# Optimization experiments

Hardware: AMD Instinct MI355X
Metric: run time of the kernel (lower is better)

The kernel has to match this reference:

```python
import jax, jax.numpy as jnp
import numpy as np

MARGIN = 0.3


def setup_inputs() -> dict:
    key = jax.random.key(0)
    k1, k2 = jax.random.split(key)
    N, D, C = 8192, 512, 1024
    embeddings = jax.random.normal(k1, (N, D), dtype=jnp.float32)
    labels = jax.random.randint(k2, (N,), 0, C, dtype=jnp.int64)
    return {"embeddings": embeddings, "labels": labels}


def reference(embeddings, labels):
    # L2-normalize rows, cosine distance via Gram matrix: d = 1 - e_i . e_j
    e = embeddings / jnp.linalg.norm(embeddings, axis=1, keepdims=True)
    dist = 1.0 - jnp.matmul(e, e.T)  # [N, N]

    same = labels[:, None] == labels[None, :]           # [N, N] bool
    eye = jnp.eye(labels.shape[0], dtype=bool)
    pos_mask = same & ~eye                              # positives exclude self
    neg_mask = ~same                                    # negatives

    # Batch-hard mining: hardest (farthest) positive, hardest (closest) negative
    hardest_pos = jnp.max(jnp.where(pos_mask, dist, -jnp.inf), axis=1)
    hardest_neg = jnp.min(jnp.where(neg_mask, dist, jnp.inf), axis=1)

    loss = jax.nn.relu(hardest_pos - hardest_neg + MARGIN)
    return jnp.mean(loss)
```

## Files before the change

kernel.cpp:

```cpp
#include <hip/hip_runtime.h>
#include <hip/hip_fp8.h>
#include <hip/hip_fp16.h>
#include <stdint.h>

#define MARGIN 0.3f

constexpr int N = 8192;
constexpr int D = 512;
constexpr int BM = 128, BN = 128;
constexpr int NKS = D / 64;
constexpr int NT = N / BM;
constexpr int NPAIR = NT * (NT + 1) / 2;
constexpr int WEDGE = NPAIR / 8;
constexpr float ESCALE = 16.0f;
constexpr float INV_SC2 = 1.0f / (ESCALE * ESCALE);

typedef int i32x8 __attribute__((ext_vector_type(8)));
typedef float f32x16 __attribute__((ext_vector_type(16)));
typedef __fp16 h2 __attribute__((ext_vector_type(2)));

constexpr unsigned INF2 = 0x7C007C00u;

__device__ __forceinline__ unsigned char f2fp8(float f) {
  return __hip_fp8_e4m3(f).__x;
}

__device__ __forceinline__ unsigned pkmin(unsigned a, unsigned b) {
  unsigned d;
  asm("v_pk_min_f16 %0, %1, %2" : "=v"(d) : "v"(a), "v"(b));
  return d;
}

__device__ __forceinline__ unsigned cvtpk(float lo, float hi) {
  union { h2 h; unsigned u; } cv;
  cv.h = __builtin_amdgcn_cvt_pkrtz(lo, hi);
  return cv.u;
}

__device__ __forceinline__ void pair_from_q(int q, int& ti, int& tj) {
  int SI = 0;
  while (32 * (SI + 1) * (SI + 1) + 4 * (SI + 1) <= q) ++SI;
  int r = q - (32 * SI * SI + 4 * SI);
  int i, j, SJ;
  if (r < 64 * SI) {
    SJ = r >> 6;
    int w = r & 63;
    i = w >> 3;
    j = w & 7;
  } else {
    int d = r - 64 * SI;
    SJ = SI;
    i = 0;
    while ((i + 1) * (i + 2) / 2 <= d) ++i;
    j = d - i * (i + 1) / 2;
  }
  ti = SI * 8 + i;
  tj = SJ * 8 + j;
}


__global__ __launch_bounds__(256) void normalize_rows(
    const float* __restrict__ emb, unsigned char* __restrict__ e8,
    float* __restrict__ out) {
  if (blockIdx.x == 0 && threadIdx.x == 0) out[0] = 0.f;
  const int wave = threadIdx.x >> 6, lane = threadIdx.x & 63;
  const int row = blockIdx.x * 4 + wave;
  const float4* src = (const float4*)(emb + (size_t)row * D);
  float4 x0 = src[lane];
  float4 x1 = src[lane + 64];
  float ss = x0.x * x0.x + x0.y * x0.y + x0.z * x0.z + x0.w * x0.w +
             x1.x * x1.x + x1.y * x1.y + x1.z * x1.z + x1.w * x1.w;
#pragma unroll
  for (int m = 1; m < 64; m <<= 1) ss += __shfl_xor(ss, m, 64);
  const float r = rsqrtf(ss) * ESCALE;
  union { unsigned char b[8]; uint2 u; } o;
  o.b[0] = f2fp8(x0.x * r); o.b[1] = f2fp8(x0.y * r);
  o.b[2] = f2fp8(x0.z * r); o.b[3] = f2fp8(x0.w * r);
  o.b[4] = f2fp8(x1.x * r); o.b[5] = f2fp8(x1.y * r);
  o.b[6] = f2fp8(x1.z * r); o.b[7] = f2fp8(x1.w * r);
  const int n = row & 31;
  const unsigned inner =
      ((unsigned)(n * 64 + ((lane >> 1) & 3) * 16) ^
       ((unsigned)((n >> 1) & 7) << 4)) + (lane & 1) * 8;
  const unsigned off = (unsigned)((row >> 5) * 8 + (lane >> 3)) * 2048 + inner;
  *(uint2*)(e8 + off) = o.u;
}

__global__ __launch_bounds__(256, 3) void bh_gemm_sym(
    const unsigned char* __restrict__ e8, const int* __restrict__ labels,
    unsigned* __restrict__ scr) {
  __shared__ unsigned char lds[2][16384];
  __shared__ unsigned bufR[2][128];
  __shared__ unsigned bufC[2][128];

  const int b = blockIdx.x;
  const int q = WEDGE * (b & 7) + (b >> 3);
  int ti, tj;
  pair_from_q(q, ti, tj);
  const int iBase = ti * BM, jBase = tj * BN;
  const bool diag = (ti == tj);

  const int tid = threadIdx.x;
  const int lane = tid & 63;
  const int wave = tid >> 6;
  const int wr = wave >> 1, wc = wave & 1;
  const int n = lane & 31, hi = lane >> 5;

  const unsigned o0 =
      (unsigned)(n * 64 + hi * 32) ^ ((unsigned)((n >> 1) & 7) << 4);

  const unsigned char* gsrc[4];
  unsigned ldst[4];
#pragma unroll
  for (int j = 0; j < 4; ++j) {
    const int id = wave * 4 + j;
    const int mat = id >> 3;
    const int fb = (id & 7) >> 1;
    const int rb = (mat ? (jBase >> 5) : (iBase >> 5)) + fb;
    gsrc[j] = e8 + (size_t)(rb * 8) * 2048 + (id & 1) * 1024 + lane * 16;
    ldst[j] = (unsigned)id * 1024 + lane * 16;
  }

  auto STAGE = [&](int T, int buf) {
#pragma unroll
    for (int j = 0; j < 4; ++j)
      __builtin_amdgcn_global_load_lds(
          (const __attribute__((address_space(1))) unsigned int*)(gsrc[j] +
                                                                  (size_t)T * 2048),
          (__attribute__((address_space(3))) unsigned int*)(&lds[buf][ldst[j]]),
          16, 0, 0);
  };

  f32x16 acc[2][2];
#pragma unroll
  for (int t = 0; t < 2; ++t)
#pragma unroll
    for (int c = 0; c < 2; ++c) acc[t][c] = (f32x16)0.0f;

  STAGE(0, 0);
  __syncthreads();
#pragma unroll
  for (int T = 0; T < NKS; ++T) {
    const int cur = T & 1;
    if (T + 1 < NKS) STAGE(T + 1, cur ^ 1);
    union { i32x8 v; int4 q2[2]; } aF[2], bF[2];
#pragma unroll
    for (int t = 0; t < 2; ++t) {
      const unsigned char* ab = &lds[cur][(wr * 2 + t) * 2048];
      aF[t].q2[0] = *(const int4*)(ab + o0);
      aF[t].q2[1] = *(const int4*)(ab + (o0 ^ 16));
      const unsigned char* bb = &lds[cur][8192 + (wc * 2 + t) * 2048];
      bF[t].q2[0] = *(const int4*)(bb + o0);
      bF[t].q2[1] = *(const int4*)(bb + (o0 ^ 16));
    }
#pragma unroll
    for (int t = 0; t < 2; ++t)
#pragma unroll
      for (int c = 0; c < 2; ++c)
        acc[t][c] = __builtin_amdgcn_mfma_scale_f32_32x32x64_f8f6f4(
            aF[t].v, bF[c].v, acc[t][c], 0, 0,
            0, 127, 0, 127);
    __syncthreads();
  }

  int lj[2];
#pragma unroll
  for (int c = 0; c < 2; ++c) lj[c] = labels[jBase + wc * 64 + c * 32 + n];

  unsigned colAcc[2] = {INF2, INF2};

#pragma unroll
  for (int t = 0; t < 2; ++t) {
    int li[16];
#pragma unroll
    for (int a = 0; a < 4; ++a) {
      int4 v = *(const int4*)(labels + iBase + wr * 64 + t * 32 + 4 * hi + 8 * a);
      li[4 * a + 0] = v.x; li[4 * a + 1] = v.y;
      li[4 * a + 2] = v.z; li[4 * a + 3] = v.w;
    }
    unsigned P[2][16];
#pragma unroll
    for (int c = 0; c < 2; ++c) {
#pragma unroll
      for (int r = 0; r < 16; ++r) {
        const float s = acc[t][c][r];
        const unsigned u = cvtpk(s, -s);
        const bool same = (li[r] == lj[c]);
        const unsigned sel = same ? 0x0000FFFFu : 0xFFFF0000u;
        unsigned p = (sel & u) | (~sel & INF2);
        if (diag) {
          const int row32 = (r & 3) + 8 * (r >> 2) + 4 * hi;
          const bool self =
              (wr * 64 + t * 32 + row32) == (wc * 64 + c * 32 + n);
          p = self ? INF2 : p;
        }
        P[c][r] = p;
      }
      if (!diag) {
        unsigned cm = P[c][0];
#pragma unroll
        for (int r = 1; r < 16; ++r) cm = pkmin(cm, P[c][r]);
        colAcc[c] = pkmin(colAcc[c], cm);
      }
    }
    unsigned m[16];
#pragma unroll
    for (int r = 0; r < 16; ++r) m[r] = pkmin(P[0][r], P[1][r]);
    unsigned w8[8];
#pragma unroll
    for (int i = 0; i < 8; ++i) {
      unsigned x = pkmin(m[2 * i],     __shfl_xor(m[2 * i],     16, 64));
      unsigned y = pkmin(m[2 * i + 1], __shfl_xor(m[2 * i + 1], 16, 64));
      w8[i] = (lane & 16) ? y : x;
    }
    unsigned w4[4];
#pragma unroll
    for (int i = 0; i < 4; ++i) {
      unsigned x = pkmin(w8[2 * i],     __shfl_xor(w8[2 * i],     8, 64));
      unsigned y = pkmin(w8[2 * i + 1], __shfl_xor(w8[2 * i + 1], 8, 64));
      w4[i] = (lane & 8) ? y : x;
    }
    unsigned w2[2];
#pragma unroll
    for (int i = 0; i < 2; ++i) {
      unsigned x = pkmin(w4[2 * i],     __shfl_xor(w4[2 * i],     4, 64));
      unsigned y = pkmin(w4[2 * i + 1], __shfl_xor(w4[2 * i + 1], 4, 64));
      w2[i] = (lane & 4) ? y : x;
    }
    unsigned x1 = pkmin(w2[0], __shfl_xor(w2[0], 2, 64));
    unsigned y1 = pkmin(w2[1], __shfl_xor(w2[1], 2, 64));
    unsigned w1 = (lane & 2) ? y1 : x1;
    w1 = pkmin(w1, __shfl_xor(w1, 1, 64));
    const int row32 = 16 * ((lane >> 1) & 1) + 8 * ((lane >> 2) & 1) + 4 * hi +
                      2 * ((lane >> 3) & 1) + ((lane >> 4) & 1);
    if ((lane & 1) == 0) bufR[wc][wr * 64 + t * 32 + row32] = w1;
  }

  if (!diag) {
#pragma unroll
    for (int c = 0; c < 2; ++c)
      colAcc[c] = pkmin(colAcc[c], __shfl_xor(colAcc[c], 32, 64));
    if (hi == 0) {
#pragma unroll
      for (int c = 0; c < 2; ++c)
        bufC[wr][wc * 64 + c * 32 + n] = colAcc[c];
    }
  }

  __syncthreads();

  if (wc == 0) {
    const int row = wr * 64 + lane;
    scr[(unsigned)(iBase + row) * 64 + tj] = pkmin(bufR[0][row], bufR[1][row]);
  }
  if (!diag && wr == 0) {
    const int col = wc * 64 + lane;
    scr[(unsigned)(jBase + col) * 64 + ti] = pkmin(bufC[0][col], bufC[1][col]);
  }
}

__global__ __launch_bounds__(256) void finalize_loss(
    const unsigned* __restrict__ scr, float* __restrict__ out) {
  const int row = blockIdx.x * 256 + threadIdx.x;
  const uint4* p = (const uint4*)(scr + (size_t)row * 64);
  unsigned mm = INF2;
#pragma unroll
  for (int i = 0; i < 16; ++i) {
    uint4 w = p[i];
    mm = pkmin(mm, pkmin(pkmin(w.x, w.y), pkmin(w.z, w.w)));
  }
  const float mn = __half2float(__ushort_as_half((unsigned short)(mm & 0xffff)));
  const float nmx = __half2float(__ushort_as_half((unsigned short)(mm >> 16)));
  float loss = (-nmx - mn) * INV_SC2 + MARGIN;
  float sum = loss > 0.f ? loss : 0.f;
#pragma unroll
  for (int m = 1; m < 64; m <<= 1) sum += __shfl_xor(sum, m, 64);
  __shared__ float ws4[4];
  const int lane = threadIdx.x & 63, wave = threadIdx.x >> 6;
  if (lane == 0) ws4[wave] = sum;
  __syncthreads();
  if (threadIdx.x == 0)
    atomicAdd(out, (ws4[0] + ws4[1] + ws4[2] + ws4[3]) * (1.0f / N));
}

extern "C" void kernel_launch(void* const* d_in, const int* in_sizes, int n_in,
                              void* d_out, int out_size, void* d_ws, size_t ws_size,
                              hipStream_t stream) {
  const float* emb = (const float*)d_in[0];
  const int* labels = (const int*)d_in[1];
  float* out = (float*)d_out;

  unsigned char* e8 = (unsigned char*)d_ws;
  unsigned* scr = (unsigned*)((char*)d_ws + (size_t)4 * 1024 * 1024);

  normalize_rows<<<N / 4, 256, 0, stream>>>(emb, e8, out);
  bh_gemm_sym<<<NPAIR, 256, 0, stream>>>(e8, labels, scr);
  finalize_loss<<<N / 256, 256, 0, stream>>>(scr, out);
}
```

Baseline: 102.6 us.

## Use ds_swizzle reductions, nontemporal stores, and hoist label loads before GEMM loop

Replaces the __shfl_xor butterfly steps in the row-min reduction with ds_swizzle bit-mode XOR patterns, which need no address computation. The column-label loads move ahead of the K loop so their latency overlaps the MFMA work. The fp8 embedding writes and the partial-min scratch writes become nontemporal stores to reduce cache pollution. The nontemporal e8 store may hurt, since the GEMM kernel rereads that data right afterwards.

```diff
diff --git a/kernel.cpp b/kernel.cpp
--- a/kernel.cpp
+++ b/kernel.cpp
@@ -73,7 +73,7 @@
 #pragma unroll
   for (int m = 1; m < 64; m <<= 1) ss += __shfl_xor(ss, m, 64);
   const float r = rsqrtf(ss) * ESCALE;
-  union { unsigned char b[8]; uint2 u; } o;
+  union { unsigned char b[8]; unsigned long long u; } o;
   o.b[0] = f2fp8(x0.x * r); o.b[1] = f2fp8(x0.y * r);
   o.b[2] = f2fp8(x0.z * r); o.b[3] = f2fp8(x0.w * r);
   o.b[4] = f2fp8(x1.x * r); o.b[5] = f2fp8(x1.y * r);
@@ -83,7 +83,7 @@
       ((unsigned)(n * 64 + ((lane >> 1) & 3) * 16) ^
        ((unsigned)((n >> 1) & 7) << 4)) + (lane & 1) * 8;
   const unsigned off = (unsigned)((row >> 5) * 8 + (lane >> 3)) * 2048 + inner;
-  *(uint2*)(e8 + off) = o.u;
+  __builtin_nontemporal_store(o.u, (unsigned long long*)(e8 + off));
 }
 
 __global__ __launch_bounds__(256, 3) void bh_gemm_sym(
@@ -131,6 +131,10 @@
           16, 0, 0);
   };
 
+  int lj[2];
+#pragma unroll
+  for (int c = 0; c < 2; ++c) lj[c] = labels[jBase + wc * 64 + c * 32 + n];
+
   f32x16 acc[2][2];
 #pragma unroll
   for (int t = 0; t < 2; ++t)
@@ -162,10 +166,6 @@
             0, 127, 0, 127);
     __syncthreads();
   }
-
-  int lj[2];
-#pragma unroll
-  for (int c = 0; c < 2; ++c) lj[c] = labels[jBase + wc * 64 + c * 32 + n];
 
   unsigned colAcc[2] = {INF2, INF2};
 
@@ -209,28 +209,36 @@
     unsigned w8[8];
 #pragma unroll
     for (int i = 0; i < 8; ++i) {
-      unsigned x = pkmin(m[2 * i],     __shfl_xor(m[2 * i],     16, 64));
-      unsigned y = pkmin(m[2 * i + 1], __shfl_xor(m[2 * i + 1], 16, 64));
+      unsigned x = pkmin(m[2 * i],
+          (unsigned)__builtin_amdgcn_ds_swizzle((int)m[2 * i], 0x401F));
+      unsigned y = pkmin(m[2 * i + 1],
+          (unsigned)__builtin_amdgcn_ds_swizzle((int)m[2 * i + 1], 0x401F));
       w8[i] = (lane & 16) ? y : x;
     }
     unsigned w4[4];
 #pragma unroll
     for (int i = 0; i < 4; ++i) {
-      unsigned x = pkmin(w8[2 * i],     __shfl_xor(w8[2 * i],     8, 64));
-      unsigned y = pkmin(w8[2 * i + 1], __shfl_xor(w8[2 * i + 1], 8, 64));
+      unsigned x = pkmin(w8[2 * i],
+          (unsigned)__builtin_amdgcn_ds_swizzle((int)w8[2 * i], 0x201F));
+      unsigned y = pkmin(w8[2 * i + 1],
+          (unsigned)__builtin_amdgcn_ds_swizzle((int)w8[2 * i + 1], 0x201F));
       w4[i] = (lane & 8) ? y : x;
     }
     unsigned w2[2];
 #pragma unroll
     for (int i = 0; i < 2; ++i) {
-      unsigned x = pkmin(w4[2 * i],     __shfl_xor(w4[2 * i],     4, 64));
-      unsigned y = pkmin(w4[2 * i + 1], __shfl_xor(w4[2 * i + 1], 4, 64));
+      unsigned x = pkmin(w4[2 * i],
+          (unsigned)__builtin_amdgcn_ds_swizzle((int)w4[2 * i], 0x101F));
+      unsigned y = pkmin(w4[2 * i + 1],
+          (unsigned)__builtin_amdgcn_ds_swizzle((int)w4[2 * i + 1], 0x101F));
       w2[i] = (lane & 4) ? y : x;
     }
-    unsigned x1 = pkmin(w2[0], __shfl_xor(w2[0], 2, 64));
-    unsigned y1 = pkmin(w2[1], __shfl_xor(w2[1], 2, 64));
+    unsigned x1 = pkmin(w2[0],
+        (unsigned)__builtin_amdgcn_ds_swizzle((int)w2[0], 0x081F));
+    unsigned y1 = pkmin(w2[1],
+        (unsigned)__builtin_amdgcn_ds_swizzle((int)w2[1], 0x081F));
     unsigned w1 = (lane & 2) ? y1 : x1;
-    w1 = pkmin(w1, __shfl_xor(w1, 1, 64));
+    w1 = pkmin(w1, (unsigned)__builtin_amdgcn_ds_swizzle((int)w1, 0x041F));
     const int row32 = 16 * ((lane >> 1) & 1) + 8 * ((lane >> 2) & 1) + 4 * hi +
                       2 * ((lane >> 3) & 1) + ((lane >> 4) & 1);
     if ((lane & 1) == 0) bufR[wc][wr * 64 + t * 32 + row32] = w1;
@@ -251,11 +259,13 @@
 
   if (wc == 0) {
     const int row = wr * 64 + lane;
-    scr[(unsigned)(iBase + row) * 64 + tj] = pkmin(bufR[0][row], bufR[1][row]);
+    __builtin_nontemporal_store(pkmin(bufR[0][row], bufR[1][row]),
+                                &scr[(unsigned)(iBase + row) * 64 + tj]);
   }
   if (!diag && wr == 0) {
     const int col = wc * 64 + lane;
-    scr[(unsigned)(jBase + col) * 64 + ti] = pkmin(bufC[0][col], bufC[1][col]);
+    __builtin_nontemporal_store(pkmin(bufC[0][col], bufC[1][col]),
+                                &scr[(unsigned)(jBase + col) * 64 + ti]);
   }
 }
 
```

Result: no change. 102.2 us, median of 2 (-0.4%).
